# Kernel optimization log

Measured on AMD Instinct MI355X. Metric: run time of the kernel, lower is better.

Reference implementation:

```python
import jax, jax.numpy as jnp
import numpy as np

T, B, I, H, A = 2048, 2, 40, 44, 262144  # seq_len, batch, input, hidden, max action len
E = 2 * H  # 88, branch embedding dim; E + I == 128 (Linear in_features)


def setup_inputs() -> dict:
    key = jax.random.key(0)
    ks = jax.random.split(key, 11)
    s = 1.0 / np.sqrt(H).astype(np.float32)
    u = lambda k, shape: jax.random.uniform(k, shape, jnp.float32, -s, s)
    sl = 1.0 / np.sqrt(E + I).astype(np.float32)
    return {
        "x": jax.random.normal(ks[0], (T, B, I), jnp.float32),
        "h0": jax.random.normal(ks[1], (1, B, H), jnp.float32),
        "c0": jax.random.normal(ks[2], (1, B, H), jnp.float32),
        "action": jax.random.normal(ks[3], (B, A, I), jnp.float32),
        "act_length": jax.random.randint(ks[4], (B,), 1, A + 1, jnp.int32),
        "W_ih": u(ks[5], (4 * H, I)),
        "W_hh": u(ks[6], (4 * H, H)),
        "b_ih": u(ks[7], (4 * H,)),
        "b_hh": u(ks[8], (4 * H,)),
        "W_v": jax.random.uniform(ks[9], (1, E + I), jnp.float32, -sl, sl),
        "b_v": jax.random.uniform(ks[10], (1,), jnp.float32, -sl, sl),
    }


def _lstm_final(x, h0, c0, W_ih, W_hh, b_ih, b_hh):
    # single-layer LSTM, returns final (h, c), each (B, H); torch gate order i,f,g,o
    def step(carry, xt):
        h, c = carry
        g = xt @ W_ih.T + b_ih + h @ W_hh.T + b_hh  # (B, 4H)
        i, f, gg, o = jnp.split(g, 4, axis=-1)
        c = jax.nn.sigmoid(f) * c + jax.nn.sigmoid(i) * jnp.tanh(gg)
        h = jax.nn.sigmoid(o) * jnp.tanh(c)
        return (h, c), None
    (h, c), _ = jax.lax.scan(step, (h0[0], c0[0]), x)
    return h, c


def reference(x, h0, c0, action, act_length, W_ih, W_hh, b_ih, b_hh, W_v, b_v):
    h, c = _lstm_final(x, h0, c0, W_ih, W_hh, b_ih, b_hh)
    emb = jnp.concatenate([h, c], axis=-1)  # (B, 88) == brench_embeding[0]
    w = W_v[0]
    w_e, w_a = w[:E], w[E:]  # split Linear(128->1) weight over [embed | act]
    # val[b, i] = emb[b].w_e + action[b, i].w_a + b_v  (fused ragged linear)
    vals = (emb @ w_e)[:, None] + jnp.einsum("bad,d->ba", action, w_a) + b_v[0]
    mask = jnp.arange(A)[None, :] < act_length[:, None]  # ragged lengths
    return jnp.where(mask, vals, 0.0)
```

## Files before the change

### kernel.cpp

```cpp
#include <hip/hip_runtime.h>

typedef float v2f __attribute__((ext_vector_type(2)));
typedef float v4f __attribute__((ext_vector_type(4)));

#define T_STEPS 2048
#define BATCH   2
#define IDIM    40
#define HDIM    44
#define GDIM    176
#define ADIM    262144
#define EDIM    88
#define NEG_L   (-1.4426950408889634f)
#define NEG_2L  (-2.8853900817779268f)

__global__ __launch_bounds__(192) void xproj_kernel(
    const float* __restrict__ x,
    const float* __restrict__ W_ih,
    const float* __restrict__ b_ih,
    const float* __restrict__ b_hh,
    float* __restrict__ xproj)
{
    const int tb = blockIdx.x;
    const int gi = threadIdx.x;
    __shared__ __align__(16) float xs[IDIM];
    if (threadIdx.x < IDIM) xs[threadIdx.x] = x[(size_t)tb * IDIM + threadIdx.x];
    __syncthreads();
    if (gi < GDIM) {
        const float* wr = W_ih + gi * IDIM;
        float a0 = 0.f, a1 = 0.f;
        #pragma unroll
        for (int i = 0; i < IDIM; i += 4) {
            float4 wv = *(const float4*)&wr[i];
            float4 xv = *(const float4*)&xs[i];
            a0 += wv.x * xv.x + wv.z * xv.z;
            a1 += wv.y * xv.y + wv.w * xv.w;
        }
        const float scale = (gi >= 2 * HDIM && gi < 3 * HDIM) ? NEG_2L : NEG_L;
        xproj[(size_t)tb * GDIM + gi] = scale * (a0 + a1 + b_ih[gi] + b_hh[gi]);
    }
}

__global__ __launch_bounds__(64)
__attribute__((amdgpu_waves_per_eu(1, 1)))
void lstm_kernel(
    const float* __restrict__ xproj,
    const float* __restrict__ h0,
    const float* __restrict__ c0,
    const float* __restrict__ W_hh,
    const float* __restrict__ W_v,
    const float* __restrict__ b_v,
    float* __restrict__ base_out)
{
    const int b = blockIdx.x;
    const int j = threadIdx.x;
    const int jj = (j < HDIM) ? j : (HDIM - 1);

    __shared__ __align__(16) float h_sh[64];

    v2f wi[22], wf[22], wg[22], wo[22];
    {
        const float* ri = W_hh + (size_t)jj * HDIM;
        const float* rf = W_hh + (size_t)(HDIM + jj) * HDIM;
        const float* rg = W_hh + (size_t)(2 * HDIM + jj) * HDIM;
        const float* ro = W_hh + (size_t)(3 * HDIM + jj) * HDIM;
        #pragma unroll
        for (int k = 0; k < 22; ++k) {
            wi[k] = ((const v2f*)ri)[k] * NEG_L;
            wf[k] = ((const v2f*)rf)[k] * NEG_L;
            wg[k] = ((const v2f*)rg)[k] * NEG_2L;
            wo[k] = ((const v2f*)ro)[k] * NEG_L;
        }
    }

    float c = c0[b * HDIM + jj];
    h_sh[j] = (j < HDIM) ? h0[b * HDIM + j] : 0.f;

    v2f hp[22];
    #pragma unroll
    for (int k = 0; k < 11; ++k) {
        v4f t = ((const v4f*)h_sh)[k];
        hp[2 * k]     = __builtin_shufflevector(t, t, 0, 1);
        hp[2 * k + 1] = __builtin_shufflevector(t, t, 2, 3);
    }

    const float* xp = xproj + (size_t)b * GDIM;
    #define LDX(dst, s) { const float* _a = xp + (size_t)(s) * (BATCH * GDIM); \
        dst##0 = _a[jj]; dst##1 = _a[HDIM + jj]; dst##2 = _a[2 * HDIM + jj]; dst##3 = _a[3 * HDIM + jj]; }
    float r0, r1, r2, r3, p0, p1, p2, p3;
    LDX(r, 0) LDX(p, 1)

    float hval = 0.f;

    #pragma unroll 1
    for (int step = 0; step < T_STEPS; ++step) {
        v2f ai0 = (v2f)(0.f), ai1 = (v2f)(0.f), af0 = (v2f)(0.f), af1 = (v2f)(0.f);
        v2f ag0 = (v2f)(0.f), ag1 = (v2f)(0.f), ao0 = (v2f)(0.f), ao1 = (v2f)(0.f);
        #pragma unroll
        for (int k = 0; k < 22; k += 2) {
            ai0 = __builtin_elementwise_fma(wi[k],     hp[k],     ai0);
            ai1 = __builtin_elementwise_fma(wi[k + 1], hp[k + 1], ai1);
            af0 = __builtin_elementwise_fma(wf[k],     hp[k],     af0);
            af1 = __builtin_elementwise_fma(wf[k + 1], hp[k + 1], af1);
            ag0 = __builtin_elementwise_fma(wg[k],     hp[k],     ag0);
            ag1 = __builtin_elementwise_fma(wg[k + 1], hp[k + 1], ag1);
            ao0 = __builtin_elementwise_fma(wo[k],     hp[k],     ao0);
            ao1 = __builtin_elementwise_fma(wo[k + 1], hp[k + 1], ao1);
        }
        v2f si2 = ai0 + ai1; float yi = si2.x + si2.y + r0;
        v2f sf2 = af0 + af1; float yf = sf2.x + sf2.y + r1;
        v2f sg2 = ag0 + ag1; float yg = sg2.x + sg2.y + r2;
        v2f so2 = ao0 + ao1; float yo = so2.x + so2.y + r3;

        float s_i = __builtin_amdgcn_rcpf(1.0f + __builtin_amdgcn_exp2f(yi));
        float s_f = __builtin_amdgcn_rcpf(1.0f + __builtin_amdgcn_exp2f(yf));
        float w_g = __builtin_amdgcn_rcpf(1.0f + __builtin_amdgcn_exp2f(yg));
        float s_o = __builtin_amdgcn_rcpf(1.0f + __builtin_amdgcn_exp2f(yo));
        float t_g = __builtin_fmaf(2.0f, w_g, -1.0f);
        c = s_f * c + s_i * t_g;
        float y_c = c * NEG_2L;
        float w_c = __builtin_amdgcn_rcpf(1.0f + __builtin_amdgcn_exp2f(y_c));
        float two_so = s_o + s_o;
        hval = __builtin_fmaf(two_so, w_c, -s_o);

        h_sh[j] = hval;
        #pragma unroll
        for (int k = 0; k < 11; ++k) {
            v4f t = ((const v4f*)h_sh)[k];
            hp[2 * k]     = __builtin_shufflevector(t, t, 0, 1);
            hp[2 * k + 1] = __builtin_shufflevector(t, t, 2, 3);
        }

        r0 = p0; r1 = p1; r2 = p2; r3 = p3;
        const int ns = (step + 2 < T_STEPS) ? step + 2 : (T_STEPS - 1);
        LDX(p, ns)
    }
    #undef LDX

    float p = 0.f;
    if (j < HDIM) p = hval * W_v[j] + c * W_v[HDIM + j];
    #pragma unroll
    for (int off = 32; off; off >>= 1) p += __shfl_down(p, off);
    if (j == 0) base_out[b] = p + b_v[0];
}

__global__ __launch_bounds__(256) void action_kernel(
    const float* __restrict__ action,
    const int*   __restrict__ act_length,
    const float* __restrict__ W_v,
    const float* __restrict__ base,
    float* __restrict__ out)
{
    const int idx = blockIdx.x * 256 + threadIdx.x;
    const int b = idx >> 18;
    const int a = idx & (ADIM - 1);
    if (a >= act_length[b]) { out[idx] = 0.f; return; }
    const float* row = action + (size_t)idx * IDIM;
    float a0 = 0.f, a1 = 0.f;
    #pragma unroll
    for (int i = 0; i < IDIM; i += 4) {
        float4 av = *(const float4*)&row[i];
        a0 += av.x * W_v[EDIM + i + 0] + av.z * W_v[EDIM + i + 2];
        a1 += av.y * W_v[EDIM + i + 1] + av.w * W_v[EDIM + i + 3];
    }
    out[idx] = base[b] + a0 + a1;
}

extern "C" void kernel_launch(void* const* d_in, const int* in_sizes, int n_in,
                              void* d_out, int out_size, void* d_ws, size_t ws_size,
                              hipStream_t stream) {
    const float* x        = (const float*)d_in[0];
    const float* h0       = (const float*)d_in[1];
    const float* c0       = (const float*)d_in[2];
    const float* action   = (const float*)d_in[3];
    const int*   act_len  = (const int*)  d_in[4];
    const float* W_ih     = (const float*)d_in[5];
    const float* W_hh     = (const float*)d_in[6];
    const float* b_ih     = (const float*)d_in[7];
    const float* b_hh     = (const float*)d_in[8];
    const float* W_v      = (const float*)d_in[9];
    const float* b_v      = (const float*)d_in[10];
    float* out = (float*)d_out;

    float* xproj = (float*)d_ws;
    float* base  = xproj + (size_t)T_STEPS * BATCH * GDIM;

    xproj_kernel<<<dim3(T_STEPS * BATCH), dim3(192), 0, stream>>>(
        x, W_ih, b_ih, b_hh, xproj);
    lstm_kernel<<<dim3(BATCH), dim3(64), 0, stream>>>(
        xproj, h0, c0, W_hh, W_v, b_v, base);
    action_kernel<<<dim3((BATCH * ADIM) / 256), dim3(256), 0, stream>>>(
        action, act_len, W_v, base, out);
}
```

Baseline: 694.6 us.

## Process both batch sequences in a single LSTM wavefront to interleave dependency chains

Merges the two per-batch LSTM blocks into one 64-thread block that advances both batch recurrences together, sharing the register-resident W_hh weights. The independent A/B chains are interleaved so their FMA, transcendental and LDS round-trip latencies can overlap within one wave. In exchange each step does twice the arithmetic in a single wave instead of two parallel CUs, and register pressure rises with the extra h vectors, which risks spills.

```diff
diff --git a/kernel.cpp b/kernel.cpp
--- a/kernel.cpp
+++ b/kernel.cpp
@@ -51,11 +51,11 @@
     const float* __restrict__ b_v,
     float* __restrict__ base_out)
 {
-    const int b = blockIdx.x;
     const int j = threadIdx.x;
     const int jj = (j < HDIM) ? j : (HDIM - 1);
 
-    __shared__ __align__(16) float h_sh[64];
+    __shared__ __align__(16) float hA_sh[64];
+    __shared__ __align__(16) float hB_sh[64];
 
     v2f wi[22], wf[22], wg[22], wo[22];
     {
@@ -72,75 +72,112 @@
         }
     }
 
-    float c = c0[b * HDIM + jj];
-    h_sh[j] = (j < HDIM) ? h0[b * HDIM + j] : 0.f;
-
-    v2f hp[22];
+    float cA = c0[jj];
+    float cB = c0[HDIM + jj];
+    hA_sh[j] = (j < HDIM) ? h0[j] : 0.f;
+    hB_sh[j] = (j < HDIM) ? h0[HDIM + j] : 0.f;
+
+    v2f hpA[22], hpB[22];
     #pragma unroll
     for (int k = 0; k < 11; ++k) {
-        v4f t = ((const v4f*)h_sh)[k];
-        hp[2 * k]     = __builtin_shufflevector(t, t, 0, 1);
-        hp[2 * k + 1] = __builtin_shufflevector(t, t, 2, 3);
-    }
-
-    const float* xp = xproj + (size_t)b * GDIM;
-    #define LDX(dst, s) { const float* _a = xp + (size_t)(s) * (BATCH * GDIM); \
+        v4f tA = ((const v4f*)hA_sh)[k];
+        hpA[2 * k]     = __builtin_shufflevector(tA, tA, 0, 1);
+        hpA[2 * k + 1] = __builtin_shufflevector(tA, tA, 2, 3);
+        v4f tB = ((const v4f*)hB_sh)[k];
+        hpB[2 * k]     = __builtin_shufflevector(tB, tB, 0, 1);
+        hpB[2 * k + 1] = __builtin_shufflevector(tB, tB, 2, 3);
+    }
+
+    const float* xpA = xproj;
+    const float* xpB = xproj + GDIM;
+    #define LDX(base, dst, s) { const float* _a = (base) + (size_t)(s) * (BATCH * GDIM); \
         dst##0 = _a[jj]; dst##1 = _a[HDIM + jj]; dst##2 = _a[2 * HDIM + jj]; dst##3 = _a[3 * HDIM + jj]; }
-    float r0, r1, r2, r3, p0, p1, p2, p3;
-    LDX(r, 0) LDX(p, 1)
-
-    float hval = 0.f;
+    float rA0, rA1, rA2, rA3, pA0, pA1, pA2, pA3;
+    float rB0, rB1, rB2, rB3, pB0, pB1, pB2, pB3;
+    LDX(xpA, rA, 0) LDX(xpA, pA, 1)
+    LDX(xpB, rB, 0) LDX(xpB, pB, 1)
+
+    float hvalA = 0.f, hvalB = 0.f;
 
     #pragma unroll 1
     for (int step = 0; step < T_STEPS; ++step) {
-        v2f ai0 = (v2f)(0.f), ai1 = (v2f)(0.f), af0 = (v2f)(0.f), af1 = (v2f)(0.f);
-        v2f ag0 = (v2f)(0.f), ag1 = (v2f)(0.f), ao0 = (v2f)(0.f), ao1 = (v2f)(0.f);
-        #pragma unroll
-        for (int k = 0; k < 22; k += 2) {
-            ai0 = __builtin_elementwise_fma(wi[k],     hp[k],     ai0);
-            ai1 = __builtin_elementwise_fma(wi[k + 1], hp[k + 1], ai1);
-            af0 = __builtin_elementwise_fma(wf[k],     hp[k],     af0);
-            af1 = __builtin_elementwise_fma(wf[k + 1], hp[k + 1], af1);
-            ag0 = __builtin_elementwise_fma(wg[k],     hp[k],     ag0);
-            ag1 = __builtin_elementwise_fma(wg[k + 1], hp[k + 1], ag1);
-            ao0 = __builtin_elementwise_fma(wo[k],     hp[k],     ao0);
-            ao1 = __builtin_elementwise_fma(wo[k + 1], hp[k + 1], ao1);
-        }
-        v2f si2 = ai0 + ai1; float yi = si2.x + si2.y + r0;
-        v2f sf2 = af0 + af1; float yf = sf2.x + sf2.y + r1;
-        v2f sg2 = ag0 + ag1; float yg = sg2.x + sg2.y + r2;
-        v2f so2 = ao0 + ao1; float yo = so2.x + so2.y + r3;
-
-        float s_i = __builtin_amdgcn_rcpf(1.0f + __builtin_amdgcn_exp2f(yi));
-        float s_f = __builtin_amdgcn_rcpf(1.0f + __builtin_amdgcn_exp2f(yf));
-        float w_g = __builtin_amdgcn_rcpf(1.0f + __builtin_amdgcn_exp2f(yg));
-        float s_o = __builtin_amdgcn_rcpf(1.0f + __builtin_amdgcn_exp2f(yo));
-        float t_g = __builtin_fmaf(2.0f, w_g, -1.0f);
-        c = s_f * c + s_i * t_g;
-        float y_c = c * NEG_2L;
-        float w_c = __builtin_amdgcn_rcpf(1.0f + __builtin_amdgcn_exp2f(y_c));
-        float two_so = s_o + s_o;
-        hval = __builtin_fmaf(two_so, w_c, -s_o);
-
-        h_sh[j] = hval;
+        v2f aiA = (v2f)(0.f), afA = (v2f)(0.f), agA = (v2f)(0.f), aoA = (v2f)(0.f);
+        v2f aiB = (v2f)(0.f), afB = (v2f)(0.f), agB = (v2f)(0.f), aoB = (v2f)(0.f);
+        #pragma unroll
+        for (int k = 0; k < 22; ++k) {
+            aiA = __builtin_elementwise_fma(wi[k], hpA[k], aiA);
+            aiB = __builtin_elementwise_fma(wi[k], hpB[k], aiB);
+            afA = __builtin_elementwise_fma(wf[k], hpA[k], afA);
+            afB = __builtin_elementwise_fma(wf[k], hpB[k], afB);
+            agA = __builtin_elementwise_fma(wg[k], hpA[k], agA);
+            agB = __builtin_elementwise_fma(wg[k], hpB[k], agB);
+            aoA = __builtin_elementwise_fma(wo[k], hpA[k], aoA);
+            aoB = __builtin_elementwise_fma(wo[k], hpB[k], aoB);
+        }
+
+        float yiA = aiA.x + aiA.y + rA0;
+        float yfA = afA.x + afA.y + rA1;
+        float ygA = agA.x + agA.y + rA2;
+        float yoA = aoA.x + aoA.y + rA3;
+        float s_iA = __builtin_amdgcn_rcpf(1.0f + __builtin_amdgcn_exp2f(yiA));
+        float s_fA = __builtin_amdgcn_rcpf(1.0f + __builtin_amdgcn_exp2f(yfA));
+        float w_gA = __builtin_amdgcn_rcpf(1.0f + __builtin_amdgcn_exp2f(ygA));
+        float s_oA = __builtin_amdgcn_rcpf(1.0f + __builtin_amdgcn_exp2f(yoA));
+        float t_gA = __builtin_fmaf(2.0f, w_gA, -1.0f);
+        cA = s_fA * cA + s_iA * t_gA;
+        float w_cA = __builtin_amdgcn_rcpf(1.0f + __builtin_amdgcn_exp2f(cA * NEG_2L));
+        hvalA = __builtin_fmaf(s_oA + s_oA, w_cA, -s_oA);
+        hA_sh[j] = hvalA;
+
+        float yiB = aiB.x + aiB.y + rB0;
+        float yfB = afB.x + afB.y + rB1;
+        float ygB = agB.x + agB.y + rB2;
+        float yoB = aoB.x + aoB.y + rB3;
+        float s_iB = __builtin_amdgcn_rcpf(1.0f + __builtin_amdgcn_exp2f(yiB));
+        float s_fB = __builtin_amdgcn_rcpf(1.0f + __builtin_amdgcn_exp2f(yfB));
+        float w_gB = __builtin_amdgcn_rcpf(1.0f + __builtin_amdgcn_exp2f(ygB));
+        float s_oB = __builtin_amdgcn_rcpf(1.0f + __builtin_amdgcn_exp2f(yoB));
+        float t_gB = __builtin_fmaf(2.0f, w_gB, -1.0f);
+        cB = s_fB * cB + s_iB * t_gB;
+        float w_cB = __builtin_amdgcn_rcpf(1.0f + __builtin_amdgcn_exp2f(cB * NEG_2L));
+        hvalB = __builtin_fmaf(s_oB + s_oB, w_cB, -s_oB);
+        hB_sh[j] = hvalB;
+
         #pragma unroll
         for (int k = 0; k < 11; ++k) {
-            v4f t = ((const v4f*)h_sh)[k];
-            hp[2 * k]     = __builtin_shufflevector(t, t, 0, 1);
-            hp[2 * k + 1] = __builtin_shufflevector(t, t, 2, 3);
-        }
-
-        r0 = p0; r1 = p1; r2 = p2; r3 = p3;
+            v4f tA = ((const v4f*)hA_sh)[k];
+            hpA[2 * k]     = __builtin_shufflevector(tA, tA, 0, 1);
+            hpA[2 * k + 1] = __builtin_shufflevector(tA, tA, 2, 3);
+        }
+        #pragma unroll
+        for (int k = 0; k < 11; ++k) {
+            v4f tB = ((const v4f*)hB_sh)[k];
+            hpB[2 * k]     = __builtin_shufflevector(tB, tB, 0, 1);
+            hpB[2 * k + 1] = __builtin_shufflevector(tB, tB, 2, 3);
+        }
+
+        rA0 = pA0; rA1 = pA1; rA2 = pA2; rA3 = pA3;
+        rB0 = pB0; rB1 = pB1; rB2 = pB2; rB3 = pB3;
         const int ns = (step + 2 < T_STEPS) ? step + 2 : (T_STEPS - 1);
-        LDX(p, ns)
+        LDX(xpA, pA, ns)
+        LDX(xpB, pB, ns)
     }
     #undef LDX
 
-    float p = 0.f;
-    if (j < HDIM) p = hval * W_v[j] + c * W_v[HDIM + j];
+    float pA = 0.f, pB = 0.f;
+    if (j < HDIM) {
+        pA = hvalA * W_v[j] + cA * W_v[HDIM + j];
+        pB = hvalB * W_v[j] + cB * W_v[HDIM + j];
+    }
     #pragma unroll
-    for (int off = 32; off; off >>= 1) p += __shfl_down(p, off);
-    if (j == 0) base_out[b] = p + b_v[0];
+    for (int off = 32; off; off >>= 1) {
+        pA += __shfl_down(pA, off);
+        pB += __shfl_down(pB, off);
+    }
+    if (j == 0) {
+        base_out[0] = pA + b_v[0];
+        base_out[1] = pB + b_v[0];
+    }
 }
 
 __global__ __launch_bounds__(256) void action_kernel(
@@ -186,7 +223,7 @@
 
     xproj_kernel<<<dim3(T_STEPS * BATCH), dim3(192), 0, stream>>>(
         x, W_ih, b_ih, b_hh, xproj);
-    lstm_kernel<<<dim3(BATCH), dim3(64), 0, stream>>>(
+    lstm_kernel<<<dim3(1), dim3(64), 0, stream>>>(
         xproj, h0, c0, W_hh, W_v, b_v, base);
     action_kernel<<<dim3((BATCH * ADIM) / 256), dim3(256), 0, stream>>>(
         action, act_len, W_v, base, out);
```

Result: slower. 1.483 ms (+113.5%).

## Split LSTM gate matvecs across two waves and lane halves with barrier sync

Applied to the files above, without the earlier changes.

Restructures the recurrent LSTM kernel from one 64-thread wave, where each lane computed all four gates for one hidden unit, to 128 threads. Each wave owns 22 hidden units, and each lane half computes two gate rows, exchanging activations via a cross-half shuffle. This cuts each lane's serial FMA chain per step from four gate dot products to two, shortening the sequential critical path. In exchange it adds a __syncthreads per timestep across two waves plus a shuffle, which may cost more than the arithmetic it saves.

```diff
diff --git a/kernel.cpp b/kernel.cpp
--- a/kernel.cpp
+++ b/kernel.cpp
@@ -40,7 +40,7 @@
     }
 }
 
-__global__ __launch_bounds__(64)
+__global__ __launch_bounds__(128)
 __attribute__((amdgpu_waves_per_eu(1, 1)))
 void lstm_kernel(
     const float* __restrict__ xproj,
@@ -51,29 +51,39 @@
     const float* __restrict__ b_v,
     float* __restrict__ base_out)
 {
-    const int b = blockIdx.x;
-    const int j = threadIdx.x;
-    const int jj = (j < HDIM) ? j : (HDIM - 1);
+    const int b    = blockIdx.x;
+    const int tid  = threadIdx.x;
+    const int wave = tid >> 6;
+    const int lane = tid & 63;
+    const int sub  = lane & 31;
+    const int half = lane >> 5;
+    const bool act = (sub < 22);
+    const int subc = act ? sub : 21;
+    const int unit = wave * 22 + subc;
 
     __shared__ __align__(16) float h_sh[64];
-
-    v2f wi[22], wf[22], wg[22], wo[22];
+    __shared__ float part[2];
+
+    const int row0 = half ? (2 * HDIM + unit) : unit;
+    const int row1 = row0 + HDIM;
+    const float sc0 = half ? NEG_2L : NEG_L;
+    const float sc1 = NEG_L;
+
+    v2f w0[22], w1[22];
     {
-        const float* ri = W_hh + (size_t)jj * HDIM;
-        const float* rf = W_hh + (size_t)(HDIM + jj) * HDIM;
-        const float* rg = W_hh + (size_t)(2 * HDIM + jj) * HDIM;
-        const float* ro = W_hh + (size_t)(3 * HDIM + jj) * HDIM;
+        const float* r0p = W_hh + (size_t)row0 * HDIM;
+        const float* r1p = W_hh + (size_t)row1 * HDIM;
         #pragma unroll
         for (int k = 0; k < 22; ++k) {
-            wi[k] = ((const v2f*)ri)[k] * NEG_L;
-            wf[k] = ((const v2f*)rf)[k] * NEG_L;
-            wg[k] = ((const v2f*)rg)[k] * NEG_2L;
-            wo[k] = ((const v2f*)ro)[k] * NEG_L;
-        }
-    }
-
-    float c = c0[b * HDIM + jj];
-    h_sh[j] = (j < HDIM) ? h0[b * HDIM + j] : 0.f;
+            w0[k] = ((const v2f*)r0p)[k] * sc0;
+            w1[k] = ((const v2f*)r1p)[k] * sc1;
+        }
+    }
+
+    float c = c0[b * HDIM + unit];
+    if (tid < HDIM) h_sh[tid] = h0[b * HDIM + tid];
+    if (tid >= HDIM && tid < 64) h_sh[tid] = 0.f;
+    __syncthreads();
 
     v2f hp[22];
     #pragma unroll
@@ -84,45 +94,43 @@
     }
 
     const float* xp = xproj + (size_t)b * GDIM;
-    #define LDX(dst, s) { const float* _a = xp + (size_t)(s) * (BATCH * GDIM); \
-        dst##0 = _a[jj]; dst##1 = _a[HDIM + jj]; dst##2 = _a[2 * HDIM + jj]; dst##3 = _a[3 * HDIM + jj]; }
-    float r0, r1, r2, r3, p0, p1, p2, p3;
-    LDX(r, 0) LDX(p, 1)
+    #define LDX(d0, d1, s) { const float* _a = xp + (size_t)(s) * (BATCH * GDIM); \
+        d0 = _a[row0]; d1 = _a[row1]; }
+    float r0v, r1v, p0v, p1v;
+    LDX(r0v, r1v, 0) LDX(p0v, p1v, 1)
 
     float hval = 0.f;
 
     #pragma unroll 1
     for (int step = 0; step < T_STEPS; ++step) {
-        v2f ai0 = (v2f)(0.f), ai1 = (v2f)(0.f), af0 = (v2f)(0.f), af1 = (v2f)(0.f);
-        v2f ag0 = (v2f)(0.f), ag1 = (v2f)(0.f), ao0 = (v2f)(0.f), ao1 = (v2f)(0.f);
-        #pragma unroll
-        for (int k = 0; k < 22; k += 2) {
-            ai0 = __builtin_elementwise_fma(wi[k],     hp[k],     ai0);
-            ai1 = __builtin_elementwise_fma(wi[k + 1], hp[k + 1], ai1);
-            af0 = __builtin_elementwise_fma(wf[k],     hp[k],     af0);
-            af1 = __builtin_elementwise_fma(wf[k + 1], hp[k + 1], af1);
-            ag0 = __builtin_elementwise_fma(wg[k],     hp[k],     ag0);
-            ag1 = __builtin_elementwise_fma(wg[k + 1], hp[k + 1], ag1);
-            ao0 = __builtin_elementwise_fma(wo[k],     hp[k],     ao0);
-            ao1 = __builtin_elementwise_fma(wo[k + 1], hp[k + 1], ao1);
-        }
-        v2f si2 = ai0 + ai1; float yi = si2.x + si2.y + r0;
-        v2f sf2 = af0 + af1; float yf = sf2.x + sf2.y + r1;
-        v2f sg2 = ag0 + ag1; float yg = sg2.x + sg2.y + r2;
-        v2f so2 = ao0 + ao1; float yo = so2.x + so2.y + r3;
-
-        float s_i = __builtin_amdgcn_rcpf(1.0f + __builtin_amdgcn_exp2f(yi));
-        float s_f = __builtin_amdgcn_rcpf(1.0f + __builtin_amdgcn_exp2f(yf));
-        float w_g = __builtin_amdgcn_rcpf(1.0f + __builtin_amdgcn_exp2f(yg));
-        float s_o = __builtin_amdgcn_rcpf(1.0f + __builtin_amdgcn_exp2f(yo));
+        v2f a0 = {r0v, 0.f}, a1 = {r1v, 0.f};
+        #pragma unroll
+        for (int k = 0; k < 22; ++k) {
+            a0 = __builtin_elementwise_fma(w0[k], hp[k], a0);
+            a1 = __builtin_elementwise_fma(w1[k], hp[k], a1);
+        }
+        float y0 = a0.x + a0.y;
+        float y1 = a1.x + a1.y;
+
+        float v0 = __builtin_amdgcn_rcpf(1.0f + __builtin_amdgcn_exp2f(y0));
+        float v1 = __builtin_amdgcn_rcpf(1.0f + __builtin_amdgcn_exp2f(y1));
+
+        float o0 = __shfl_xor(v0, 32);
+        float o1 = __shfl_xor(v1, 32);
+
+        float s_i = half ? o0 : v0;
+        float s_f = half ? o1 : v1;
+        float w_g = half ? v0 : o0;
+        float s_o = half ? v1 : o1;
+
         float t_g = __builtin_fmaf(2.0f, w_g, -1.0f);
         c = s_f * c + s_i * t_g;
-        float y_c = c * NEG_2L;
-        float w_c = __builtin_amdgcn_rcpf(1.0f + __builtin_amdgcn_exp2f(y_c));
-        float two_so = s_o + s_o;
-        hval = __builtin_fmaf(two_so, w_c, -s_o);
-
-        h_sh[j] = hval;
+        float w_c = __builtin_amdgcn_rcpf(1.0f + __builtin_amdgcn_exp2f(c * NEG_2L));
+        hval = __builtin_fmaf(s_o + s_o, w_c, -s_o);
+
+        if (act && half == 0) h_sh[unit] = hval;
+        __syncthreads();
+
         #pragma unroll
         for (int k = 0; k < 11; ++k) {
             v4f t = ((const v4f*)h_sh)[k];
@@ -130,17 +138,19 @@
             hp[2 * k + 1] = __builtin_shufflevector(t, t, 2, 3);
         }
 
-        r0 = p0; r1 = p1; r2 = p2; r3 = p3;
+        r0v = p0v; r1v = p1v;
         const int ns = (step + 2 < T_STEPS) ? step + 2 : (T_STEPS - 1);
-        LDX(p, ns)
+        LDX(p0v, p1v, ns)
     }
     #undef LDX
 
     float p = 0.f;
-    if (j < HDIM) p = hval * W_v[j] + c * W_v[HDIM + j];
+    if (act && half == 0) p = hval * W_v[unit] + c * W_v[HDIM + unit];
     #pragma unroll
     for (int off = 32; off; off >>= 1) p += __shfl_down(p, off);
-    if (j == 0) base_out[b] = p + b_v[0];
+    if (lane == 0) part[wave] = p;
+    __syncthreads();
+    if (tid == 0) base_out[b] = part[0] + part[1] + b_v[0];
 }
 
 __global__ __launch_bounds__(256) void action_kernel(
@@ -186,7 +196,7 @@
 
     xproj_kernel<<<dim3(T_STEPS * BATCH), dim3(192), 0, stream>>>(
         x, W_ih, b_ih, b_hh, xproj);
-    lstm_kernel<<<dim3(BATCH), dim3(64), 0, stream>>>(
+    lstm_kernel<<<dim3(BATCH), dim3(128), 0, stream>>>(
         xproj, h0, c0, W_hh, W_v, b_v, base);
     action_kernel<<<dim3((BATCH * ADIM) / 256), dim3(256), 0, stream>>>(
         action, act_len, W_v, base, out);
```

Result: faster. 641.3 us (-7.7%).
